# Kernel optimization log

Hardware: AMD Instinct MI355X
Metric: run time of the kernel (lower is better)

## Reference

```python
import jax, jax.numpy as jnp
import numpy as np

N = 100000      # nodes
E = 3200000     # edges (avg degree 32)
G = 2048        # graphs in batch
F_IN = 4        # node feature dim (hardcoded in GCN.__init__)
H = 64          # hidden_dim default


def setup_inputs() -> dict:
    key = jax.random.key(0)
    ks = jax.random.split(key, 9)
    x = jax.random.normal(ks[0], (N, F_IN), dtype=jnp.float32)
    edge_index = jax.random.randint(ks[1], (2, E), 0, N, dtype=jnp.int64)
    batch = jnp.sort(jax.random.randint(ks[2], (N,), 0, G, dtype=jnp.int64))
    # learned params (Glorot-ish scaling)
    W1 = jax.random.normal(ks[3], (F_IN, H), dtype=jnp.float32) * (1.0 / np.sqrt(F_IN))
    b1 = jnp.zeros((H,), jnp.float32)
    W2 = jax.random.normal(ks[4], (H, H), dtype=jnp.float32) * (1.0 / np.sqrt(H))
    b2 = jnp.zeros((H,), jnp.float32)
    Wlin = jax.random.normal(ks[5], (H, 1), dtype=jnp.float32) * (1.0 / np.sqrt(H))
    blin = jnp.zeros((1,), jnp.float32)
    return {"x": x, "edge_index": edge_index, "batch": batch,
            "W1": W1, "b1": b1, "W2": W2, "b2": b2, "Wlin": Wlin, "blin": blin}


def _gcn_conv(x, W, b, src, dst, n):
    # PyG GCNConv: add self-loops, symmetric normalization D^-1/2 A_hat D^-1/2,
    # x' = x @ W, out[dst] += norm * x'[src], plus bias.
    xw = x @ W                                            # [N, H]
    deg = jnp.zeros((n,), xw.dtype).at[dst].add(1.0) + 1.0  # in-degree incl. self-loop
    dinv = jax.lax.rsqrt(deg)                             # deg^{-1/2}
    coef = (dinv[src] * dinv[dst])[:, None]               # [E, 1]
    agg = jax.ops.segment_sum(xw[src] * coef, dst, num_segments=n)  # neighbor msgs
    out = agg + xw * (1.0 / deg)[:, None]                 # self-loop contribution
    return out + b


def _global_mean_pool(x, batch, g):
    sums = jax.ops.segment_sum(x, batch, num_segments=g)
    cnt = jax.ops.segment_sum(jnp.ones((x.shape[0],), x.dtype), batch, num_segments=g)
    return sums / jnp.maximum(cnt, 1.0)[:, None]


def reference(x, edge_index, batch, W1, b1, W2, b2, Wlin, blin):
    src, dst = edge_index[0], edge_index[1]
    h = jax.nn.relu(_gcn_conv(x, W1, b1, src, dst, N))
    h = jax.nn.relu(_gcn_conv(h, W2, b2, src, dst, N))
    p = _global_mean_pool(h, batch, G)                    # [G, H]
    return p @ Wlin + blin                                # [G, 1]
```

## Files before the change

kernel.cpp:

```cpp
#include <hip/hip_runtime.h>
#include <hip/hip_fp16.h>

#define NN 100000
#define NE 3200000
#define NG 2048
#define HD 64
#define BUKSZ 256
#define NBUK 391
#define NB 512
#define CHUNK 6250
#define CAP 9216


typedef __attribute__((ext_vector_type(8))) _Float16 f16x8;
typedef __attribute__((ext_vector_type(4))) float f32x4;
union I4H8 { int4 i4; f16x8 h8; };


__global__ void init_k(int* __restrict__ bcur) {
    int t = blockIdx.x * blockDim.x + threadIdx.x;
    if (t <= NBUK) bcur[t] = t * CAP;
}


__global__ void w2t_k(const float* __restrict__ W2, _Float16* __restrict__ W2t) {
    int t = blockIdx.x * blockDim.x + threadIdx.x;
    if (t < HD * HD) {
        int n = t >> 6, k = t & 63;
        W2t[n * HD + k] = (_Float16)W2[k * HD + n];
    }
}


__global__ __launch_bounds__(512) void stageA_k(
        const int* __restrict__ src, const int* __restrict__ dst,
        int* __restrict__ bcur, unsigned int* __restrict__ edges2) {
    __shared__ int hist[NBUK];
    __shared__ int exb[NBUK + 1];
    __shared__ int cur[NBUK];
    __shared__ int obase[NBUK];
    __shared__ int sc[512];
    __shared__ unsigned int svals[CHUNK];
    __shared__ unsigned short sbuk[CHUNK];
    int b = blockIdx.x, t = threadIdx.x;
    int base = b * CHUNK;
    for (int i = t; i < NBUK; i += 512) hist[i] = 0;
    __syncthreads();
    for (int i = t; i < CHUNK; i += 512)
        atomicAdd(&hist[dst[base + i] >> 8], 1);
    __syncthreads();
    int v = (t < NBUK) ? hist[t] : 0;
    sc[t] = v;
    __syncthreads();
    for (int o = 1; o < 512; o <<= 1) {
        int u = (t >= o) ? sc[t - o] : 0;
        __syncthreads();
        sc[t] += u;
        __syncthreads();
    }
    if (t < NBUK) {
        int excl = sc[t] - v;
        exb[t] = excl;
        cur[t] = excl;
        obase[t] = v ? atomicAdd(&bcur[t], v) : 0;
    }
    if (t == 0) exb[NBUK] = CHUNK;
    __syncthreads();
    for (int i = t; i < CHUNK; i += 512) {
        int d = dst[base + i];
        int s = src[base + i];
        int bk = d >> 8;
        int pos = atomicAdd(&cur[bk], 1);
        svals[pos] = ((unsigned int)(d & 255) << 17) | (unsigned int)s;
        sbuk[pos] = (unsigned short)bk;
    }
    __syncthreads();
    for (int i = t; i < CHUNK; i += 512) {
        int lo = (int)sbuk[i];
        edges2[obase[lo] + (i - exb[lo])] = svals[i];
    }
}


__global__ __launch_bounds__(512) void build1_k(
        const int* __restrict__ bcur, const float4* __restrict__ x,
        unsigned int* __restrict__ edges2, int* __restrict__ row_beg,
        int* __restrict__ row_deg, float* __restrict__ dinv,
        float4* __restrict__ xs) {
    __shared__ unsigned int ebuf[CAP];
    __shared__ int deg[BUKSZ];
    __shared__ int sc[BUKSZ];
    __shared__ int cur[BUKSZ];
    int k = blockIdx.x, t = threadIdx.x;
    int base = k * CAP;
    int len = bcur[k] - base;
    if (t < BUKSZ) deg[t] = 0;
    __syncthreads();
    for (int i = t; i < len; i += 512) {
        unsigned int pv = edges2[base + i];
        ebuf[i] = pv;
        atomicAdd(&deg[pv >> 17], 1);
    }
    __syncthreads();
    int v = 0;
    if (t < BUKSZ) { v = deg[t]; sc[t] = v; }
    __syncthreads();
    for (int o = 1; o < BUKSZ; o <<= 1) {
        int u = 0;
        if (t < BUKSZ && t >= o) u = sc[t - o];
        __syncthreads();
        if (t < BUKSZ && t >= o) sc[t] += u;
        __syncthreads();
    }
    if (t < BUKSZ) {
        int excl = sc[t] - v;
        cur[t] = excl;
        int node = k * BUKSZ + t;
        if (node < NN) {
            row_beg[node] = base + excl;
            row_deg[node] = v;
            float di = rsqrtf((float)v + 1.0f);
            dinv[node] = di;
            float4 xv = x[node];
            xs[node] = make_float4(xv.x * di, xv.y * di, xv.z * di, xv.w * di);
        }
    }
    __syncthreads();
    for (int i = t; i < len; i += 512) {
        unsigned int pv = ebuf[i];
        int pos = atomicAdd(&cur[pv >> 17], 1);
        edges2[base + pos] = pv & 0x1FFFFu;
    }
}


__global__ __launch_bounds__(256) void g1f_k(
        const float4* __restrict__ xs, const unsigned int* __restrict__ csr,
        const int* __restrict__ row_beg, const int* __restrict__ row_deg,
        const float* __restrict__ dinv, const float* __restrict__ W1,
        const float* __restrict__ b1, __half* __restrict__ h1) {
    int wid = (blockIdx.x * blockDim.x + threadIdx.x) >> 6;
    int lane = threadIdx.x & 63;
    if (wid >= NN) return;
    int beg = row_beg[wid], deg = row_deg[wid];
    float sx = 0.f, sy = 0.f, sz = 0.f, sw = 0.f;
    for (int e = beg + lane; e < beg + deg; e += 64) {
        float4 w = xs[csr[e]];
        sx += w.x; sy += w.y; sz += w.z; sw += w.w;
    }
#pragma unroll
    for (int o = 1; o < 64; o <<= 1) {
        sx += __shfl_xor(sx, o);
        sy += __shfl_xor(sy, o);
        sz += __shfl_xor(sz, o);
        sw += __shfl_xor(sw, o);
    }
    float di = dinv[wid];
    float4 self = xs[wid];
    float ax = (sx + self.x) * di;
    float ay = (sy + self.y) * di;
    float az = (sz + self.z) * di;
    float aw = (sw + self.w) * di;
    float v = ax * W1[lane] + ay * W1[64 + lane] + az * W1[128 + lane] + aw * W1[192 + lane] + b1[lane];
    v = fmaxf(v, 0.f) * di;
    h1[(size_t)wid * HD + lane] = __float2half_rn(v);
}


union H8 { int4 i4; __half2 h2[4]; };

__device__ __forceinline__ __half2 shfl_xor_h2(__half2 a, int m) {
    int v = *(int*)&a;
    int s = __shfl_xor(v, m);
    return *(__half2*)&s;
}

__global__ __launch_bounds__(256) void gather2_k(
        const __half* __restrict__ h1, const unsigned int* __restrict__ csr,
        const int* __restrict__ row_beg, const int* __restrict__ row_deg,
        __half* __restrict__ a2h) {
    __shared__ int sidx[4][64];
    int wv = threadIdx.x >> 6;
    int wid = (blockIdx.x * blockDim.x + threadIdx.x) >> 6;
    int lane = threadIdx.x & 63;
    if (wid >= NN) return;
    int half = lane >> 5;
    int g = (lane >> 3) & 3;
    int sub = lane & 7;
    int hg = half * 4 + g;
    int beg = row_beg[wid], deg = row_deg[wid];
    __half2 acc[4];
#pragma unroll
    for (int j = 0; j < 4; ++j) acc[j] = __half2half2(__float2half(0.f));
    int done = 0;
    while (done < deg) {
        int chunk = deg - done;
        if (chunk > 64) chunk = 64;
        if (lane < chunk) sidx[wv][lane] = (int)csr[beg + done + lane];
        int kb = 0;
        for (; kb + 31 < chunk; kb += 32) {
            int e0 = sidx[wv][kb + hg];
            int e1 = sidx[wv][kb + hg + 8];
            int e2 = sidx[wv][kb + hg + 16];
            int e3 = sidx[wv][kb + hg + 24];
            H8 r0, r1, r2, r3;
            r0.i4 = *(const int4*)(h1 + (size_t)e0 * HD + sub * 8);
            r1.i4 = *(const int4*)(h1 + (size_t)e1 * HD + sub * 8);
            r2.i4 = *(const int4*)(h1 + (size_t)e2 * HD + sub * 8);
            r3.i4 = *(const int4*)(h1 + (size_t)e3 * HD + sub * 8);
#pragma unroll
            for (int j = 0; j < 4; ++j) {
                acc[j] = __hadd2(acc[j], __hadd2(__hadd2(r0.h2[j], r1.h2[j]),
                                                 __hadd2(r2.h2[j], r3.h2[j])));
            }
        }
        for (; kb + 7 < chunk; kb += 8) {
            int e0 = sidx[wv][kb + hg];
            H8 r0;
            r0.i4 = *(const int4*)(h1 + (size_t)e0 * HD + sub * 8);
#pragma unroll
            for (int j = 0; j < 4; ++j) acc[j] = __hadd2(acc[j], r0.h2[j]);
        }
        if (kb < chunk) {
            int e = kb + hg;
            if (e < chunk) {
                int e0 = sidx[wv][e];
                H8 r0;
                r0.i4 = *(const int4*)(h1 + (size_t)e0 * HD + sub * 8);
#pragma unroll
                for (int j = 0; j < 4; ++j) acc[j] = __hadd2(acc[j], r0.h2[j]);
            }
        }
        done += chunk;
    }
#pragma unroll
    for (int j = 0; j < 4; ++j) {
        acc[j] = __hadd2(acc[j], shfl_xor_h2(acc[j], 8));
        acc[j] = __hadd2(acc[j], shfl_xor_h2(acc[j], 16));
        acc[j] = __hadd2(acc[j], shfl_xor_h2(acc[j], 32));
    }
    if (half == 0 && g == 0) {
        H8 sv, o;
        sv.i4 = *(const int4*)(h1 + (size_t)wid * HD + sub * 8);
#pragma unroll
        for (int j = 0; j < 4; ++j) o.h2[j] = __hadd2(acc[j], sv.h2[j]);
        ((int4*)a2h)[(size_t)wid * 8 + sub] = o.i4;
    }
}


__global__ __launch_bounds__(256) void c2mfma_k(
        const __half* __restrict__ a2h, const _Float16* __restrict__ W2t,
        const float* __restrict__ b2, const float* __restrict__ dinv,
        const int* __restrict__ batch, float* __restrict__ pool) {
    int tid = threadIdx.x;
    int wave = tid >> 6, lane = tid & 63;
    int base = blockIdx.x * 64 + wave * 16;
    int m = lane & 15, kb = lane >> 4;
    f16x8 bfr[2][4];
#pragma unroll
    for (int kt = 0; kt < 2; ++kt)
#pragma unroll
        for (int nt = 0; nt < 4; ++nt) {
            I4H8 u;
            u.i4 = *(const int4*)(W2t + (nt * 16 + m) * HD + kt * 32 + kb * 8);
            bfr[kt][nt] = u.h8;
        }
    f16x8 afr[2];
    int anode = base + m;
#pragma unroll
    for (int kt = 0; kt < 2; ++kt) {
        I4H8 u;
        if (anode < NN)
            u.i4 = *(const int4*)(a2h + (size_t)anode * HD + kt * 32 + kb * 8);
        else
            u.i4 = make_int4(0, 0, 0, 0);
        afr[kt] = u.h8;
    }
    f32x4 acc[4] = {{0.f, 0.f, 0.f, 0.f}, {0.f, 0.f, 0.f, 0.f},
                    {0.f, 0.f, 0.f, 0.f}, {0.f, 0.f, 0.f, 0.f}};
#pragma unroll
    for (int kt = 0; kt < 2; ++kt)
#pragma unroll
        for (int nt = 0; nt < 4; ++nt)
            acc[nt] = __builtin_amdgcn_mfma_f32_16x16x32_f16(afr[kt], bfr[kt][nt], acc[nt], 0, 0, 0);
    int r0 = base + kb * 4;
    float dv[4];
    int bg[4];
#pragma unroll
    for (int r = 0; r < 4; ++r) {
        int node = r0 + r;
        dv[r] = (node < NN) ? dinv[node] : 0.f;
        bg[r] = (node < NN) ? batch[node] : -1;
    }
#pragma unroll
    for (int nt = 0; nt < 4; ++nt) {
        int n = nt * 16 + m;
        float bv = b2[n];
        int g = -1;
        float accf = 0.f;
#pragma unroll
        for (int r = 0; r < 4; ++r) {
            if (bg[r] < 0) break;
            float v = fmaxf(fmaf(dv[r], acc[nt][r], bv), 0.f);
            if (bg[r] != g) {
                if (g >= 0) atomicAdd(&pool[g * HD + n], accf);
                accf = 0.f; g = bg[r];
            }
            accf += v;
        }
        if (g >= 0) atomicAdd(&pool[g * HD + n], accf);
    }
}

__device__ __forceinline__ int lb_dev(const int* __restrict__ b, int n, int key) {
    int lo = 0, hi = n;
    while (lo < hi) {
        int mid = (lo + hi) >> 1;
        if (b[mid] < key) lo = mid + 1; else hi = mid;
    }
    return lo;
}

__global__ void final_k(const float* __restrict__ pool, const int* __restrict__ batch,
                        const float* __restrict__ Wlin, const float* __restrict__ blin,
                        float* __restrict__ out) {
    int g = blockIdx.x;
    int lane = threadIdx.x;
    int lo = lb_dev(batch, NN, g);
    int hi = lb_dev(batch, NN, g + 1);
    float cnt = (float)(hi - lo);
    float v = pool[g * HD + lane] * Wlin[lane];
#pragma unroll
    for (int off = 32; off > 0; off >>= 1) v += __shfl_down(v, off);
    if (lane == 0) out[g] = v / fmaxf(cnt, 1.0f) + blin[0];
}


extern "C" void kernel_launch(void* const* d_in, const int* in_sizes, int n_in,
                              void* d_out, int out_size, void* d_ws, size_t ws_size,
                              hipStream_t stream) {
    const float* x    = (const float*)d_in[0];
    const int*   ei   = (const int*)d_in[1];
    const int*   bat  = (const int*)d_in[2];
    const float* W1   = (const float*)d_in[3];
    const float* b1   = (const float*)d_in[4];
    const float* W2   = (const float*)d_in[5];
    const float* b2   = (const float*)d_in[6];
    const float* Wlin = (const float*)d_in[7];
    const float* blin = (const float*)d_in[8];
    float* out = (float*)d_out;

    const int* src = ei;
    const int* dst = ei + NE;

    char* ws = (char*)d_ws;
    size_t off = 0;
    auto alloc = [&](size_t bytes) {
        char* p = ws + off;
        off += (bytes + 255) & ~(size_t)255;
        return p;
    };
    int*   bcur    = (int*)  alloc((NBUK + 1) * sizeof(int));
    int*   row_beg = (int*)  alloc(NN * sizeof(int));
    int*   row_deg = (int*)  alloc(NN * sizeof(int));
    float* dinv    = (float*)alloc(NN * sizeof(float));
    unsigned int* edges2 = (unsigned int*)alloc((size_t)NBUK * CAP * sizeof(unsigned int));
    float4* xs     = (float4*)alloc((size_t)NN * sizeof(float4));
    __half* h1     = (__half*)alloc((size_t)NN * HD * sizeof(__half));
    __half* a2h    = (__half*)alloc((size_t)NN * HD * sizeof(__half));
    _Float16* W2t  = (_Float16*)alloc(HD * HD * sizeof(_Float16));
    float* pool    = (float*)alloc((size_t)NG * HD * sizeof(float));
    (void)ws_size; (void)n_in; (void)in_sizes; (void)out_size;

    const int BLK = 256;
    const int gW = (NN * 64 + BLK - 1) / BLK;

    init_k<<<(NBUK + 1 + 255) / 256, 256, 0, stream>>>(bcur);
    w2t_k<<<16, 256, 0, stream>>>(W2, W2t);
    stageA_k<<<NB, 512, 0, stream>>>(src, dst, bcur, edges2);
    build1_k<<<NBUK, 512, 0, stream>>>(bcur, (const float4*)x, edges2,
                                       row_beg, row_deg, dinv, xs);

    g1f_k<<<gW, BLK, 0, stream>>>(xs, edges2, row_beg, row_deg, dinv, W1, b1, h1);

    gather2_k<<<gW, BLK, 0, stream>>>(h1, edges2, row_beg, row_deg, a2h);

    hipMemsetAsync(pool, 0, (size_t)NG * HD * sizeof(float), stream);
    c2mfma_k<<<(NN + 63) / 64, 256, 0, stream>>>(a2h, W2t, b2, dinv, bat, pool);
    final_k<<<NG, 64, 0, stream>>>(pool, bat, Wlin, blin, out);
}
```

Measured before the change: 176.6 us.

## Split hidden features into four column chunks for cache-friendly layer-2 gather

```diff
diff --git a/kernel.cpp b/kernel.cpp
--- a/kernel.cpp
+++ b/kernel.cpp
@@ -138,7 +138,7 @@
         const float4* __restrict__ xs, const unsigned int* __restrict__ csr,
         const int* __restrict__ row_beg, const int* __restrict__ row_deg,
         const float* __restrict__ dinv, const float* __restrict__ W1,
-        const float* __restrict__ b1, __half* __restrict__ h1) {
+        const float* __restrict__ b1, __half* __restrict__ h1c) {
     int wid = (blockIdx.x * blockDim.x + threadIdx.x) >> 6;
     int lane = threadIdx.x & 63;
     if (wid >= NN) return;
@@ -163,7 +163,7 @@
     float aw = (sw + self.w) * di;
     float v = ax * W1[lane] + ay * W1[64 + lane] + az * W1[128 + lane] + aw * W1[192 + lane] + b1[lane];
     v = fmaxf(v, 0.f) * di;
-    h1[(size_t)wid * HD + lane] = __float2half_rn(v);
+    h1c[(size_t)(lane >> 4) * NN * 16 + (size_t)wid * 16 + (lane & 15)] = __float2half_rn(v);
 }
 
 
@@ -175,82 +175,67 @@
     return *(__half2*)&s;
 }
 
-__global__ __launch_bounds__(256) void gather2_k(
-        const __half* __restrict__ h1, const unsigned int* __restrict__ csr,
+__global__ __launch_bounds__(256) void g2c_k(
+        const __half* __restrict__ h1c, const unsigned int* __restrict__ csr,
         const int* __restrict__ row_beg, const int* __restrict__ row_deg,
-        __half* __restrict__ a2h) {
+        __half* __restrict__ a2c) {
     __shared__ int sidx[4][64];
     int wv = threadIdx.x >> 6;
-    int wid = (blockIdx.x * blockDim.x + threadIdx.x) >> 6;
+    int c = blockIdx.x & 3;
+    int nd = (blockIdx.x >> 2) * 4 + wv;
     int lane = threadIdx.x & 63;
-    if (wid >= NN) return;
-    int half = lane >> 5;
-    int g = (lane >> 3) & 3;
-    int sub = lane & 7;
-    int hg = half * 4 + g;
-    int beg = row_beg[wid], deg = row_deg[wid];
+    if (nd >= NN) return;
+    const __half* hc = h1c + (size_t)c * NN * 16;
+    int es = lane >> 1, p = lane & 1;
+    int beg = row_beg[nd], deg = row_deg[nd];
     __half2 acc[4];
 #pragma unroll
     for (int j = 0; j < 4; ++j) acc[j] = __half2half2(__float2half(0.f));
     int done = 0;
     while (done < deg) {
-        int chunk = deg - done;
-        if (chunk > 64) chunk = 64;
-        if (lane < chunk) sidx[wv][lane] = (int)csr[beg + done + lane];
+        int csz = deg - done;
+        if (csz > 64) csz = 64;
+        if (lane < csz) sidx[wv][lane] = (int)csr[beg + done + lane];
         int kb = 0;
-        for (; kb + 31 < chunk; kb += 32) {
-            int e0 = sidx[wv][kb + hg];
-            int e1 = sidx[wv][kb + hg + 8];
-            int e2 = sidx[wv][kb + hg + 16];
-            int e3 = sidx[wv][kb + hg + 24];
-            H8 r0, r1, r2, r3;
-            r0.i4 = *(const int4*)(h1 + (size_t)e0 * HD + sub * 8);
-            r1.i4 = *(const int4*)(h1 + (size_t)e1 * HD + sub * 8);
-            r2.i4 = *(const int4*)(h1 + (size_t)e2 * HD + sub * 8);
-            r3.i4 = *(const int4*)(h1 + (size_t)e3 * HD + sub * 8);
-#pragma unroll
-            for (int j = 0; j < 4; ++j) {
-                acc[j] = __hadd2(acc[j], __hadd2(__hadd2(r0.h2[j], r1.h2[j]),
-                                                 __hadd2(r2.h2[j], r3.h2[j])));
-            }
-        }
-        for (; kb + 7 < chunk; kb += 8) {
-            int e0 = sidx[wv][kb + hg];
+        for (; kb + 31 < csz; kb += 32) {
+            int e0 = sidx[wv][kb + es];
             H8 r0;
-            r0.i4 = *(const int4*)(h1 + (size_t)e0 * HD + sub * 8);
+            r0.i4 = *(const int4*)(hc + (size_t)e0 * 16 + p * 8);
 #pragma unroll
             for (int j = 0; j < 4; ++j) acc[j] = __hadd2(acc[j], r0.h2[j]);
         }
-        if (kb < chunk) {
-            int e = kb + hg;
-            if (e < chunk) {
-                int e0 = sidx[wv][e];
+        if (kb < csz) {
+            int ei = kb + es;
+            if (ei < csz) {
+                int e0 = sidx[wv][ei];
                 H8 r0;
-                r0.i4 = *(const int4*)(h1 + (size_t)e0 * HD + sub * 8);
+                r0.i4 = *(const int4*)(hc + (size_t)e0 * 16 + p * 8);
 #pragma unroll
                 for (int j = 0; j < 4; ++j) acc[j] = __hadd2(acc[j], r0.h2[j]);
             }
         }
-        done += chunk;
+        done += csz;
     }
 #pragma unroll
     for (int j = 0; j < 4; ++j) {
+        acc[j] = __hadd2(acc[j], shfl_xor_h2(acc[j], 2));
+        acc[j] = __hadd2(acc[j], shfl_xor_h2(acc[j], 4));
         acc[j] = __hadd2(acc[j], shfl_xor_h2(acc[j], 8));
         acc[j] = __hadd2(acc[j], shfl_xor_h2(acc[j], 16));
         acc[j] = __hadd2(acc[j], shfl_xor_h2(acc[j], 32));
     }
-    if (half == 0 && g == 0) {
+    if (lane < 2) {
         H8 sv, o;
-        sv.i4 = *(const int4*)(h1 + (size_t)wid * HD + sub * 8);
+        sv.i4 = *(const int4*)(hc + (size_t)nd * 16 + p * 8);
 #pragma unroll
         for (int j = 0; j < 4; ++j) o.h2[j] = __hadd2(acc[j], sv.h2[j]);
-        ((int4*)a2h)[(size_t)wid * 8 + sub] = o.i4;
+        *(int4*)(a2c + (size_t)c * NN * 16 + (size_t)nd * 16 + p * 8) = o.i4;
     }
 }
 
 
 __global__ __launch_bounds__(256) void c2mfma_k(
-        const __half* __restrict__ a2h, const _Float16* __restrict__ W2t,
+        const __half* __restrict__ a2c, const _Float16* __restrict__ W2t,
         const float* __restrict__ b2, const float* __restrict__ dinv,
         const int* __restrict__ batch, float* __restrict__ pool) {
     int tid = threadIdx.x;
@@ -271,8 +256,9 @@
 #pragma unroll
     for (int kt = 0; kt < 2; ++kt) {
         I4H8 u;
+        int cc = kt * 2 + (kb >> 1);
         if (anode < NN)
-            u.i4 = *(const int4*)(a2h + (size_t)anode * HD + kt * 32 + kb * 8);
+            u.i4 = *(const int4*)(a2c + (size_t)cc * NN * 16 + (size_t)anode * 16 + (kb & 1) * 8);
         else
             u.i4 = make_int4(0, 0, 0, 0);
         afr[kt] = u.h8;
@@ -367,8 +353,8 @@
     float* dinv    = (float*)alloc(NN * sizeof(float));
     unsigned int* edges2 = (unsigned int*)alloc((size_t)NBUK * CAP * sizeof(unsigned int));
     float4* xs     = (float4*)alloc((size_t)NN * sizeof(float4));
-    __half* h1     = (__half*)alloc((size_t)NN * HD * sizeof(__half));
-    __half* a2h    = (__half*)alloc((size_t)NN * HD * sizeof(__half));
+    __half* h1c    = (__half*)alloc((size_t)NN * HD * sizeof(__half));
+    __half* a2c    = (__half*)alloc((size_t)NN * HD * sizeof(__half));
     _Float16* W2t  = (_Float16*)alloc(HD * HD * sizeof(_Float16));
     float* pool    = (float*)alloc((size_t)NG * HD * sizeof(float));
     (void)ws_size; (void)n_in; (void)in_sizes; (void)out_size;
@@ -382,11 +368,11 @@
     build1_k<<<NBUK, 512, 0, stream>>>(bcur, (const float4*)x, edges2,
                                        row_beg, row_deg, dinv, xs);
 
-    g1f_k<<<gW, BLK, 0, stream>>>(xs, edges2, row_beg, row_deg, dinv, W1, b1, h1);
-
-    gather2_k<<<gW, BLK, 0, stream>>>(h1, edges2, row_beg, row_deg, a2h);
+    g1f_k<<<gW, BLK, 0, stream>>>(xs, edges2, row_beg, row_deg, dinv, W1, b1, h1c);
+
+    g2c_k<<<((NN + 3) / 4) * 4, BLK, 0, stream>>>(h1c, edges2, row_beg, row_deg, a2c);
 
     hipMemsetAsync(pool, 0, (size_t)NG * HD * sizeof(float), stream);
-    c2mfma_k<<<(NN + 63) / 64, 256, 0, stream>>>(a2h, W2t, b2, dinv, bat, pool);
+    c2mfma_k<<<(NN + 63) / 64, 256, 0, stream>>>(a2c, W2t, b2, dinv, bat, pool);
     final_k<<<NG, 64, 0, stream>>>(pool, bat, Wlin, blin, out);
 }
```

Result: slower. 247.0 us (+39.8%).
